# Performance work log

Hardware: AMD Instinct MI355X
Metric: run time of the kernel (lower is better)

The kernel has to match this reference:

```python
import jax, jax.numpy as jnp
import numpy as np

B = 16384
INPUT_DIM = 2048
HIDDEN = 1536
N_COMP = 256
N_LAYERS = 32
TOP_K = 4


def setup_inputs() -> dict:
    key = jax.random.key(0)
    ks = jax.random.split(key, 12)
    s_in = 1.0 / np.sqrt(INPUT_DIM)
    s_h = 1.0 / np.sqrt(HIDDEN)
    s_3 = 1.0 / np.sqrt(3)
    return {
        "x": jax.random.normal(ks[0], (B, INPUT_DIM), dtype=jnp.float32),
        "layer_idx": 3,
        "embed": jax.random.normal(ks[1], (N_LAYERS, INPUT_DIM), dtype=jnp.float32),
        "enc_w1": jax.random.uniform(ks[2], (INPUT_DIM, HIDDEN), jnp.float32, -s_in, s_in),
        "enc_b1": jax.random.uniform(ks[3], (HIDDEN,), jnp.float32, -s_in, s_in),
        "enc_w2": jax.random.uniform(ks[4], (HIDDEN, N_COMP), jnp.float32, -s_h, s_h),
        "enc_b2": jax.random.uniform(ks[5], (N_COMP,), jnp.float32, -s_h, s_h),
        "components": jax.random.normal(ks[6], (N_COMP, 3), dtype=jnp.float32),
        "dec_w1": jax.random.uniform(ks[7], (3, HIDDEN), jnp.float32, -s_3, s_3),
        "dec_b1": jax.random.uniform(ks[8], (HIDDEN,), jnp.float32, -s_3, s_3),
        "dec_w2": jax.random.uniform(ks[9], (HIDDEN, INPUT_DIM), jnp.float32, -s_h, s_h),
        "dec_b2": jax.random.uniform(ks[10], (INPUT_DIM,), jnp.float32, -s_h, s_h),
    }


def reference(x, layer_idx, embed, enc_w1, enc_b1, enc_w2, enc_b2,
              components, dec_w1, dec_b1, dec_w2, dec_b2):
    # x: (B, D). Add per-layer embedding row.
    x = x + embed[layer_idx]
    # Encoder MLP: Linear -> GELU (exact, erf-based like torch default) -> Linear
    h = jax.nn.gelu(x @ enc_w1 + enc_b1, approximate=False)
    logits = h @ enc_w2 + enc_b2                     # (B, C)
    # Top-k gated masked softmax: softmax over only the top_k logits per row.
    vals, idx = jax.lax.top_k(logits, TOP_K)         # (B, K), (B, K)
    w = jax.nn.softmax(vals, axis=-1)                # (B, K)
    # Sparse mix: equivalent to masked_fill(-inf) softmax @ components
    pts = jnp.einsum('bk,bkc->bc', w, components[idx])  # (B, 3)
    # Decoder MLP
    d = jax.nn.gelu(pts @ dec_w1 + dec_b1, approximate=False)
    decoded = d @ dec_w2 + dec_b2                    # (B, D)
    encoded = jnp.broadcast_to(components[None], (x.shape[0], N_COMP, 3))
    return encoded, decoded
```

## Files before the change

kernel.cpp:

```cpp
#include <hip/hip_runtime.h>


typedef float  f32x4  __attribute__((ext_vector_type(4)));
typedef short  short8 __attribute__((ext_vector_type(8)));
typedef int    i32x4  __attribute__((ext_vector_type(4)));

#define DEVINL __device__ __forceinline__

constexpr int  NB      = 16384;
constexpr int  IN_DIM  = 2048;
constexpr int  HID     = 1536;
constexpr int  NC      = 256;
constexpr long ENC_ELEMS = (long)NB * NC * 3;
constexpr float TAU  = 2e-5f;
constexpr float TAU1 = 1.5e-3f;
constexpr int  MAXR  = 64;
constexpr int  M2CAP = 2048;
constexpr int  NKT1 = IN_DIM / 32;
constexpr int  NKT2 = HID / 32;

constexpr float SCALE_X  = 3251.2f;
constexpr float SCALE_W1 = 1471325.0f;
constexpr float SCALE_H  = 4644.5714f;
constexpr float SCALE_W2 = 1274205.0f;
constexpr double INV_S1 = 1.0 / ((double)SCALE_X * (double)SCALE_W1);
constexpr double INV_S2 = 1.0 / ((double)SCALE_H * (double)SCALE_W2);
constexpr float C_DA     = 3.0f;
constexpr float SCALE_DA = 39.08f;
constexpr float SCALE_W2D = 4977.0f;
constexpr double INV_SD = 1.0 / ((double)SCALE_DA * (double)SCALE_W2D);

DEVINL unsigned short f2bf(float f) {
  unsigned int u = __builtin_bit_cast(unsigned int, f);
  u = u + 0x7fffu + ((u >> 16) & 1u);
  return (unsigned short)(u >> 16);
}
DEVINL float bf2f(unsigned short h) {
  unsigned int u = ((unsigned int)h) << 16;
  return __builtin_bit_cast(float, u);
}
DEVINL float gelu_f(float v) {
  return 0.5f * v * (1.0f + erff(v * 0.70710678118654752440f));
}
DEVINL void llds16(const void* g, void* l) {
  __builtin_amdgcn_global_load_lds(
      (const __attribute__((address_space(1))) void*)g,
      (__attribute__((address_space(3))) void*)l, 16, 0, 0);
}
DEVINL f32x4 mfma_bf16(short8 a, short8 b, f32x4 c) {
  return __builtin_amdgcn_mfma_f32_16x16x32_bf16(a, b, c, 0, 0, 0);
}
DEVINL i32x4 mfma_i8(i32x4 a, i32x4 b, i32x4 c) {
  return __builtin_amdgcn_mfma_i32_16x16x64_i8(a, b, c, 0, 0, 0);
}
DEVINL long packed_off(long tileIdx, int rowp, int kq, int e) {
  int slot = kq ^ ((rowp >> 1) & 3);
  return (tileIdx * 512 + rowp * 4 + slot) * 8 + e;
}
DEVINL int swz_idx(int rowp, int kq) {
  return (rowp * 4 + (kq ^ ((rowp >> 1) & 3))) * 8;
}
DEVINL long i8_off(long tile64, int rowp, int kin64) {
  return tile64 * 8192 + rowp * 64 + kin64;
}
DEVINL int quant16(float v, float scale) {
  int q = (int)lrintf(v * scale);
  if (q >  32512) q =  32512;
  if (q < -32512) q = -32512;
  return q;
}
DEVINL int quant8(float v, float scale) {
  int q = (int)lrintf(v * scale);
  if (q >  127) q =  127;
  if (q < -127) q = -127;
  return q;
}

__global__ __launch_bounds__(256) void mega_prep_kernel(
    const float* __restrict__ W1, const float* __restrict__ W2,
    const float* __restrict__ W2d, const float* __restrict__ b2d,
    const float* __restrict__ x, const float* __restrict__ embedMat,
    const int* __restrict__ liPtr,
    unsigned short* __restrict__ W1hT, unsigned short* __restrict__ W1lT,
    unsigned short* __restrict__ W2hT, unsigned short* __restrict__ W2lT,
    char* __restrict__ W1qh, char* __restrict__ W1ql,
    char* __restrict__ W2qh, char* __restrict__ W2ql,
    char* __restrict__ W2dq, float* __restrict__ badj,
    char* __restrict__ Xh, char* __restrict__ Xl,
    int* __restrict__ cnt, int* __restrict__ cnt2)
{
  constexpr int E0 = 3072;
  constexpr int E1 = E0 + 384;
  constexpr int E2 = E1 + 3072;
  constexpr int E3 = E2 + 8;
  constexpr int E4 = E3 + 8192;
  int b = blockIdx.x;
  int tid = threadIdx.x;
  __shared__ float t[32][33];

  if (b < E1) {
    const float* in; int N, nktB, nkt64; float qscale;
    unsigned short *oH, *oL; char *qH, *qL;
    int bx, by;
    if (b < E0) { in = W1;  N = HID; nktB = NKT1; nkt64 = IN_DIM / 64;
                  qscale = SCALE_W1; oH = W1hT; oL = W1lT; qH = W1qh; qL = W1ql;
                  bx = b % 48; by = b / 48; }
    else        { int bb = b - E0;
                  in = W2;  N = NC;  nktB = NKT2; nkt64 = HID / 64;
                  qscale = SCALE_W2; oH = W2hT; oL = W2lT; qH = W2qh; qL = W2ql;
                  bx = bb % 8; by = bb / 8; }
    int tx = tid & 31, ty = tid >> 5;
    int n0 = bx * 32, k0 = by * 32;
#pragma unroll
    for (int i = 0; i < 4; ++i)
      t[ty + i * 8][tx] = in[(long)(k0 + ty + i * 8) * N + n0 + tx];
    __syncthreads();
    int n = n0 + tx;
    int j = ty & 3;
    {
      long off = packed_off((long)(n >> 7) * nktB + (k0 >> 5), n & 127, j, 0);
      if (ty < 4) {
        short8 hv;
#pragma unroll
        for (int e = 0; e < 8; ++e) hv[e] = (short)f2bf(t[j * 8 + e][tx]);
        *(short8*)(oH + off) = hv;
      } else {
        short8 lv;
#pragma unroll
        for (int e = 0; e < 8; ++e) {
          float f = t[j * 8 + e][tx];
          lv[e] = (short)f2bf(f - bf2f(f2bf(f)));
        }
        *(short8*)(oL + off) = lv;
      }
    }
    {
      int kb = k0 + j * 8;
      long off = i8_off((long)(n >> 7) * nkt64 + (kb >> 6), n & 127, kb & 63);
      union { char b[8]; long v; } u;
      if (ty < 4) {
#pragma unroll
        for (int e = 0; e < 8; ++e) {
          int q = quant16(t[j * 8 + e][tx], qscale);
          int lo = (q << 24) >> 24;
          u.b[e] = (char)((q - lo) >> 8);
        }
        *(long*)(qH + off) = u.v;
      } else {
#pragma unroll
        for (int e = 0; e < 8; ++e) {
          int q = quant16(t[j * 8 + e][tx], qscale);
          u.b[e] = (char)((q << 24) >> 24);
        }
        *(long*)(qL + off) = u.v;
      }
    }
  } else if (b < E2) {
    int bb = b - E1;
    int bx = bb % 64, by = bb / 64;
    int tx = tid & 31, ty = tid >> 5;
    int n0 = bx * 32, k0 = by * 32;
#pragma unroll
    for (int i = 0; i < 4; ++i)
      t[ty + i * 8][tx] = W2d[(long)(k0 + ty + i * 8) * IN_DIM + n0 + tx];
    __syncthreads();
    if (ty < 4) {
      int n = n0 + tx;
      int kb = k0 + ty * 8;
      long off = i8_off((long)(n >> 7) * (HID / 64) + (kb >> 6), n & 127, kb & 63);
      union { char b[8]; long v; } u;
#pragma unroll
      for (int e = 0; e < 8; ++e)
        u.b[e] = (char)quant8(t[ty * 8 + e][tx], SCALE_W2D);
      *(long*)(W2dq + off) = u.v;
    }
  } else if (b < E3) {
    int j = (b - E2) * 256 + tid;
    float s = 0.f;
    for (int k = 0; k < HID; ++k) s += W2d[(long)k * IN_DIM + j];
    badj[j] = b2d[j] + C_DA * s;
  } else if (b < E4) {
    long g = (long)(b - E3) * 256 + tid;
    int row = (int)(g >> 7);
    int k0 = ((int)(g & 127)) * 16;
    int li = liPtr[0];
    const float* xr = x + (long)row * IN_DIM + k0;
    const float* er = embedMat + (long)li * IN_DIM + k0;
    union { char b[16]; i32x4 v; } hu, lu;
#pragma unroll
    for (int c = 0; c < 4; ++c) {
      f32x4 a = *(const f32x4*)(xr + c * 4);
      f32x4 e = *(const f32x4*)(er + c * 4);
#pragma unroll
      for (int jj = 0; jj < 4; ++jj) {
        int q = quant16(a[jj] + e[jj], SCALE_X);
        int lo = (q << 24) >> 24;
        hu.b[c * 4 + jj] = (char)((q - lo) >> 8);
        lu.b[c * 4 + jj] = (char)lo;
      }
    }
    long off = i8_off((long)(row >> 7) * (IN_DIM / 64) + (k0 >> 6), row & 127, k0 & 63);
    *(i32x4*)(Xh + off) = hu.v;
    *(i32x4*)(Xl + off) = lu.v;
  } else {
    if (tid == 0) { *cnt = 0; *cnt2 = 0; }
  }
}

template<int OUT, int PRODUCTS>
__global__ __launch_bounds__(256, 2) void gemm_i8_kernel(
    const char* __restrict__ Ah, const char* __restrict__ Al,
    const char* __restrict__ Bh, const char* __restrict__ Bl,
    int nkt64, const float* __restrict__ bias, double invScale,
    float* __restrict__ Cf, long ldc,
    char* __restrict__ Qh, char* __restrict__ Ql, int nktOut64, float outScale,
    int nbn)
{
  __shared__ alignas(16) char sAh[8192];
  __shared__ alignas(16) char sAl[PRODUCTS == 3 ? 8192 : 16];
  __shared__ alignas(16) char sBh[8192];
  __shared__ alignas(16) char sBl[PRODUCTS == 3 ? 8192 : 16];
  __shared__ float sBias[128];

  int tid = threadIdx.x;
  int nwg = gridDim.x, q = nwg >> 3, b0 = blockIdx.x;
  int sw = (b0 & 7) * q + (b0 >> 3);
  int bm = sw / nbn, bn = sw % nbn;

  if (tid < 128) sBias[tid] = bias[bn * 128 + tid];

  int wid = tid >> 6, lane = tid & 63;
  int wm = wid >> 1, wn = wid & 1;
  int l15 = lane & 15, kq = lane >> 4;

  i32x4 accH[4][4] = {};
  i32x4 accM[4][4] = {};

  for (int kt = 0; kt < nkt64; ++kt) {
    __syncthreads();
    {
      const char* g0 = Ah + ((long)(bm * nkt64 + kt)) * 8192 + tid * 16;
      llds16(g0, sAh + tid * 16); llds16(g0 + 4096, sAh + 4096 + tid * 16);
      const char* g2 = Bh + ((long)(bn * nkt64 + kt)) * 8192 + tid * 16;
      llds16(g2, sBh + tid * 16); llds16(g2 + 4096, sBh + 4096 + tid * 16);
      if constexpr (PRODUCTS == 3) {
        const char* g1 = Al + ((long)(bm * nkt64 + kt)) * 8192 + tid * 16;
        llds16(g1, sAl + tid * 16); llds16(g1 + 4096, sAl + 4096 + tid * 16);
        const char* g3 = Bl + ((long)(bn * nkt64 + kt)) * 8192 + tid * 16;
        llds16(g3, sBl + tid * 16); llds16(g3 + 4096, sBl + 4096 + tid * 16);
      }
    }
    __syncthreads();

    i32x4 bhf[4], blf[4];
#pragma unroll
    for (int n = 0; n < 4; ++n) {
      int off = (wn * 64 + n * 16 + l15) * 64 + kq * 16;
      bhf[n] = *(const i32x4*)&sBh[off];
      if constexpr (PRODUCTS == 3) blf[n] = *(const i32x4*)&sBl[off];
    }
#pragma unroll
    for (int m = 0; m < 4; ++m) {
      int off = (wm * 64 + m * 16 + l15) * 64 + kq * 16;
      i32x4 ahf = *(const i32x4*)&sAh[off];
      i32x4 alf;
      if constexpr (PRODUCTS == 3) alf = *(const i32x4*)&sAl[off];
#pragma unroll
      for (int n = 0; n < 4; ++n) {
        accH[m][n] = mfma_i8(ahf, bhf[n], accH[m][n]);
        if constexpr (PRODUCTS == 3) {
          accM[m][n] = mfma_i8(alf, bhf[n], accM[m][n]);
          accM[m][n] = mfma_i8(ahf, blf[n], accM[m][n]);
        }
      }
    }
  }

#pragma unroll
  for (int m = 0; m < 4; ++m) {
#pragma unroll
    for (int n = 0; n < 4; ++n) {
      int  gcol = bn * 128 + wn * 64 + n * 16 + l15;
      float bb  = sBias[wn * 64 + n * 16 + l15];
#pragma unroll
      for (int r = 0; r < 4; ++r) {
        long grow = (long)bm * 128 + wm * 64 + m * 16 + kq * 4 + r;
        double dv;
        if constexpr (PRODUCTS == 3)
          dv = (double)accH[m][n][r] * 65536.0 + (double)accM[m][n][r] * 256.0;
        else
          dv = (double)accH[m][n][r];
        float v = (float)(dv * invScale) + bb;
        if constexpr (OUT == 0) {
          Cf[grow * ldc + gcol] = v;
        } else {
          v = gelu_f(v);
          int qq = quant16(v, outScale);
          int lo = (qq << 24) >> 24;
          long off = i8_off((long)(grow >> 7) * nktOut64 + (gcol >> 6),
                            (int)(grow & 127), gcol & 63);
          Qh[off] = (char)((qq - lo) >> 8);
          Ql[off] = (char)lo;
        }
      }
    }
  }
}

template<bool SPLIT, int OUT_MODE, bool GELU, int KU>
__global__ __launch_bounds__(256) void gemm2_kernel(
    const unsigned short* __restrict__ Ah, const unsigned short* __restrict__ Al,
    const unsigned short* __restrict__ Bh, const unsigned short* __restrict__ Bl,
    int nkt, const float* __restrict__ bias, float* __restrict__ Cf,
    unsigned short* __restrict__ Ch, unsigned short* __restrict__ Cl,
    long ldc, int nktOut, int nbn, const int* __restrict__ mrows, int mcap)
{
  __shared__ alignas(16) unsigned short sAh[4096 * KU];
  __shared__ alignas(16) unsigned short sAl[SPLIT ? 4096 * KU : 8];
  __shared__ alignas(16) unsigned short sBh[4096 * KU];
  __shared__ alignas(16) unsigned short sBl[SPLIT ? 4096 * KU : 8];
  __shared__ float sBias[128];

  int tid = threadIdx.x;
  int nwg = gridDim.x, q = nwg >> 3, b0 = blockIdx.x;
  int sw = (b0 & 7) * q + (b0 >> 3);
  int bm = sw / nbn, bn = sw % nbn;

  if (mrows) {
    int v = *mrows; if (v > mcap) v = mcap;
    if (bm * 128 >= v) return;
  }

  if (tid < 128) sBias[tid] = bias[bn * 128 + tid];

  int wid = tid >> 6, lane = tid & 63;
  int wm = wid >> 1, wn = wid & 1;
  int l15 = lane & 15, kq = lane >> 4;

  f32x4 acc[4][4] = {};

  for (int kt = 0; kt < nkt; kt += KU) {
    __syncthreads();
#pragma unroll
    for (int u = 0; u < KU; ++u) {
      {
        const char* gA = (const char*)Ah + ((long)(bm * nkt + kt + u)) * 8192 + tid * 16;
        llds16(gA,        (char*)sAh + u * 8192 + tid * 16);
        llds16(gA + 4096, (char*)sAh + u * 8192 + 4096 + tid * 16);
      }
      if constexpr (SPLIT) {
        const char* gA = (const char*)Al + ((long)(bm * nkt + kt + u)) * 8192 + tid * 16;
        llds16(gA,        (char*)sAl + u * 8192 + tid * 16);
        llds16(gA + 4096, (char*)sAl + u * 8192 + 4096 + tid * 16);
      }
      {
        const char* gB = (const char*)Bh + ((long)(bn * nkt + kt + u)) * 8192 + tid * 16;
        llds16(gB,        (char*)sBh + u * 8192 + tid * 16);
        llds16(gB + 4096, (char*)sBh + u * 8192 + 4096 + tid * 16);
      }
      if constexpr (SPLIT) {
        const char* gB = (const char*)Bl + ((long)(bn * nkt + kt + u)) * 8192 + tid * 16;
        llds16(gB,        (char*)sBl + u * 8192 + tid * 16);
        llds16(gB + 4096, (char*)sBl + u * 8192 + 4096 + tid * 16);
      }
    }
    __syncthreads();

#pragma unroll
    for (int u = 0; u < KU; ++u) {
      short8 bh[4], bl[4];
#pragma unroll
      for (int n = 0; n < 4; ++n) {
        int idx = u * 4096 + swz_idx(wn * 64 + n * 16 + l15, kq);
        bh[n] = *(const short8*)&sBh[idx];
        if constexpr (SPLIT) bl[n] = *(const short8*)&sBl[idx];
      }
#pragma unroll
      for (int m = 0; m < 4; ++m) {
        int idx = u * 4096 + swz_idx(wm * 64 + m * 16 + l15, kq);
        short8 ah = *(const short8*)&sAh[idx];
        short8 al;
        if constexpr (SPLIT) al = *(const short8*)&sAl[idx];
#pragma unroll
        for (int n = 0; n < 4; ++n) {
          acc[m][n] = mfma_bf16(ah, bh[n], acc[m][n]);
          if constexpr (SPLIT) {
            acc[m][n] = mfma_bf16(al, bh[n], acc[m][n]);
            acc[m][n] = mfma_bf16(ah, bl[n], acc[m][n]);
          }
        }
      }
    }
  }

#pragma unroll
  for (int m = 0; m < 4; ++m) {
#pragma unroll
    for (int n = 0; n < 4; ++n) {
      int  gcol = bn * 128 + wn * 64 + n * 16 + l15;
      float bb  = sBias[wn * 64 + n * 16 + l15];
#pragma unroll
      for (int r = 0; r < 4; ++r) {
        long grow = (long)bm * 128 + wm * 64 + m * 16 + kq * 4 + r;
        float v = acc[m][n][r] + bb;
        if constexpr (GELU) v = gelu_f(v);
        if constexpr (OUT_MODE == 0) {
          Cf[grow * ldc + gcol] = v;
        } else {
          int Mt = (int)(grow >> 7), rowpo = (int)(grow & 127);
          int Kt = gcol >> 5, kqo = (gcol >> 3) & 3, e = gcol & 7;
          long off = packed_off((long)Mt * nktOut + Kt, rowpo, kqo, e);
          unsigned short hb = f2bf(v);
          Ch[off] = hb;
          Cl[off] = f2bf(v - bf2f(hb));
        }
      }
    }
  }
}

__global__ __launch_bounds__(256) void topk_screen_kernel(
    const float* __restrict__ logits, const float* __restrict__ comp,
    float* __restrict__ pts, float* __restrict__ encOut,
    int* __restrict__ cnt2, int* __restrict__ list2,
    int* __restrict__ rescueCnt, int* __restrict__ rescueList)
{
  int wid = threadIdx.x >> 6, lane = threadIdx.x & 63;
  long row = (long)blockIdx.x * 4 + wid;
  f32x4 v4 = *(const f32x4*)(logits + row * NC + lane * 4);
  float a[4] = {v4[0], v4[1], v4[2], v4[3]};

  float tv[5]; int ti[5];
#pragma unroll
  for (int t = 0; t < 5; ++t) {
    float lv = a[0]; int li = lane * 4;
#pragma unroll
    for (int i = 1; i < 4; ++i)
      if (a[i] > lv) { lv = a[i]; li = lane * 4 + i; }
#pragma unroll
    for (int off = 32; off >= 1; off >>= 1) {
      float ov = __shfl_xor(lv, off);
      int   oi = __shfl_xor(li, off);
      if (ov > lv || (ov == lv && oi < li)) { lv = ov; li = oi; }
    }
    tv[t] = lv; ti[t] = li;
    if (t < 4 && (li >> 2) == lane) a[li & 3] = -INFINITY;
  }

  bool flag = (tv[3] - tv[4]) < TAU1;
  if (!flag) {
    float m = tv[0], w[4], s = 0.f;
#pragma unroll
    for (int t = 0; t < 4; ++t) { w[t] = expf(tv[t] - m); s += w[t]; }
    float inv = 1.0f / s;
    if (lane < 3) {
      float p = 0.f;
#pragma unroll
      for (int t = 0; t < 4; ++t) p += w[t] * inv * comp[ti[t] * 3 + lane];
      pts[row * 3 + lane] = p;
    }
  } else if (lane == 0) {
    int pos = atomicAdd(cnt2, 1);
    if (pos < M2CAP) list2[pos] = (int)row;
    else { int rp = atomicAdd(rescueCnt, 1); rescueList[rp] = (int)row; }
  }

  const f32x4* cv = (const f32x4*)comp;
  f32x4* ov = (f32x4*)encOut + (long)blockIdx.x * 768;
  for (int j = threadIdx.x; j < 768; j += 256)
    ov[j] = cv[j % 192];
}

__global__ __launch_bounds__(256) void gather_kernel(
    const float* __restrict__ x, const float* __restrict__ embedMat,
    const int* __restrict__ liPtr, const int* __restrict__ cnt2,
    const int* __restrict__ list2,
    unsigned short* __restrict__ A2h, unsigned short* __restrict__ A2l)
{
  int i = blockIdx.x;
  int c2 = *cnt2; if (c2 > M2CAP) c2 = M2CAP;
  if (i >= c2) return;
  int row = list2[i];
  int li = liPtr[0];
  int t = threadIdx.x;
  int k0 = t * 8;
  const float* xr = x + (long)row * IN_DIM + k0;
  const float* er = embedMat + (long)li * IN_DIM + k0;
  short8 hv, lv;
#pragma unroll
  for (int c = 0; c < 2; ++c) {
    f32x4 a = *(const f32x4*)(xr + c * 4);
    f32x4 e = *(const f32x4*)(er + c * 4);
#pragma unroll
    for (int jj = 0; jj < 4; ++jj) {
      float f = a[jj] + e[jj];
      unsigned short hb = f2bf(f);
      hv[c * 4 + jj] = (short)hb;
      lv[c * 4 + jj] = (short)f2bf(f - bf2f(hb));
    }
  }
  long off = packed_off((long)(i >> 7) * NKT1 + (k0 >> 5), i & 127, (k0 >> 3) & 3, 0);
  *(short8*)(A2h + off) = hv;
  *(short8*)(A2l + off) = lv;
}

__global__ __launch_bounds__(256) void topk_final_kernel(
    const float* __restrict__ logits2, const float* __restrict__ comp,
    const int* __restrict__ cnt2, const int* __restrict__ list2,
    float* __restrict__ pts, int* __restrict__ rescueCnt, int* __restrict__ rescueList)
{
  int wid = threadIdx.x >> 6, lane = threadIdx.x & 63;
  int slot = blockIdx.x * 4 + wid;
  int c2 = *cnt2; if (c2 > M2CAP) c2 = M2CAP;
  if (slot >= c2) return;
  int row = list2[slot];
  f32x4 v4 = *(const f32x4*)(logits2 + (long)slot * NC + lane * 4);
  float a[4] = {v4[0], v4[1], v4[2], v4[3]};

  float tv[5]; int ti[5];
#pragma unroll
  for (int t = 0; t < 5; ++t) {
    float lv = a[0]; int li = lane * 4;
#pragma unroll
    for (int i = 1; i < 4; ++i)
      if (a[i] > lv) { lv = a[i]; li = lane * 4 + i; }
#pragma unroll
    for (int off = 32; off >= 1; off >>= 1) {
      float ov = __shfl_xor(lv, off);
      int   oi = __shfl_xor(li, off);
      if (ov > lv || (ov == lv && oi < li)) { lv = ov; li = oi; }
    }
    tv[t] = lv; ti[t] = li;
    if (t < 4 && (li >> 2) == lane) a[li & 3] = -INFINITY;
  }

  float m = tv[0], w[4], s = 0.f;
#pragma unroll
  for (int t = 0; t < 4; ++t) { w[t] = expf(tv[t] - m); s += w[t]; }
  float inv = 1.0f / s;
  if (lane < 3) {
    float p = 0.f;
#pragma unroll
    for (int t = 0; t < 4; ++t) p += w[t] * inv * comp[ti[t] * 3 + lane];
    pts[(long)row * 3 + lane] = p;
  }
  if (lane == 0 && (tv[3] - tv[4]) < TAU) {
    int pos = atomicAdd(rescueCnt, 1);
    rescueList[pos] = row;
  }
}

__global__ __launch_bounds__(256) void rescue_h1_kernel(
    const float* __restrict__ x, const float* __restrict__ embedMat,
    const int* __restrict__ liPtr, const float* __restrict__ W1,
    const int* __restrict__ cnt, const int* __restrict__ list,
    double* __restrict__ partial)
{
  int b = blockIdx.x;
  int s = b / 24, rem = b % 24;
  int cc = rem >> 2, kp = rem & 3;
  int n = *cnt;
  if (s >= n || s >= MAXR) return;
  int row = list[s];
  __shared__ double xd[512];
  int tid = threadIdx.x;
  int li = liPtr[0];
  int k0 = kp * 512;
  for (int j = tid; j < 512; j += 256)
    xd[j] = (double)x[(long)row * IN_DIM + k0 + j]
          + (double)embedMat[(long)li * IN_DIM + k0 + j];
  __syncthreads();
  int c = cc * 256 + tid;
  const float* wp = W1 + (long)k0 * HID + c;
  double s0 = 0, s1 = 0, s2 = 0, s3 = 0;
  for (int k = 0; k < 512; k += 4) {
    s0 += xd[k]     * (double)wp[(long)k * HID];
    s1 += xd[k + 1] * (double)wp[(long)(k + 1) * HID];
    s2 += xd[k + 2] * (double)wp[(long)(k + 2) * HID];
    s3 += xd[k + 3] * (double)wp[(long)(k + 3) * HID];
  }
  partial[((long)(s * 6 + cc) * 4 + kp) * 256 + tid] = (s0 + s1) + (s2 + s3);
}

__global__ __launch_bounds__(256) void rescue_logits_kernel(
    const float* __restrict__ b1, const float* __restrict__ W2,
    const float* __restrict__ b2, const float* __restrict__ comp,
    const int* __restrict__ cnt, const int* __restrict__ list,
    const double* __restrict__ partial, float* __restrict__ pts)
{
  int s = blockIdx.x;
  int n = *cnt;
  if (s >= n || s >= MAXR) return;
  __shared__ double hd[HID];
  __shared__ double ld[NC];
  int tid = threadIdx.x;
  for (int cc = 0; cc < 6; ++cc) {
    long base = ((long)(s * 6 + cc) * 4) * 256 + tid;
    double v = (double)b1[cc * 256 + tid]
             + ((partial[base] + partial[base + 256])
              + (partial[base + 512] + partial[base + 768]));
    hd[cc * 256 + tid] = 0.5 * v * (1.0 + erf(v * 0.70710678118654752440));
  }
  __syncthreads();
  {
    const float* wp = W2 + tid;
    double a0 = 0, a1 = 0, a2 = 0, a3 = 0;
    for (int k = 0; k < HID; k += 4) {
      a0 += hd[k]     * (double)wp[(long)k * NC];
      a1 += hd[k + 1] * (double)wp[(long)(k + 1) * NC];
      a2 += hd[k + 2] * (double)wp[(long)(k + 2) * NC];
      a3 += hd[k + 3] * (double)wp[(long)(k + 3) * NC];
    }
    ld[tid] = (double)b2[tid] + ((a0 + a1) + (a2 + a3));
  }
  __syncthreads();
  if (tid == 0) {
    int row = list[s];
    int idx[4]; double val[4];
    unsigned long long mask[4] = {0, 0, 0, 0};
    for (int t = 0; t < 4; ++t) {
      double bv = -1e300; int bi = 0;
      for (int j = 0; j < NC; ++j) {
        if ((mask[j >> 6] >> (j & 63)) & 1ull) continue;
        if (ld[j] > bv) { bv = ld[j]; bi = j; }
      }
      idx[t] = bi; val[t] = bv; mask[bi >> 6] |= 1ull << (bi & 63);
    }
    double m = val[0], w[4], sum = 0;
    for (int t = 0; t < 4; ++t) { w[t] = exp(val[t] - m); sum += w[t]; }
    for (int c = 0; c < 3; ++c) {
      double p = 0;
      for (int t = 0; t < 4; ++t) p += (w[t] / sum) * (double)comp[idx[t] * 3 + c];
      pts[(long)row * 3 + c] = (float)p;
    }
  }
}

__global__ __launch_bounds__(256) void rescue_slow_kernel(
    const float* __restrict__ x, const float* __restrict__ embedMat,
    const int* __restrict__ liPtr, const float* __restrict__ W1,
    const float* __restrict__ b1, const float* __restrict__ W2,
    const float* __restrict__ b2, const float* __restrict__ comp,
    float* __restrict__ pts, const int* __restrict__ cnt, const int* __restrict__ list)
{
  __shared__ double xd[IN_DIM];
  __shared__ double hd[HID];
  __shared__ double ld[NC];
  int tid = threadIdx.x;
  int li = liPtr[0];
  int n = *cnt;
  for (int it = MAXR + blockIdx.x; it < n; it += gridDim.x) {
    int row = list[it];
    const float* xr = x + (long)row * IN_DIM;
    const float* er = embedMat + (long)li * IN_DIM;
    for (int j = tid; j < IN_DIM; j += 256)
      xd[j] = (double)xr[j] + (double)er[j];
    __syncthreads();
    for (int c = tid; c < HID; c += 256) {
      double s0 = 0, s1 = 0, s2 = 0, s3 = 0;
      const float* wp = W1 + c;
      for (int k = 0; k < IN_DIM; k += 4) {
        s0 += xd[k]     * (double)wp[(long)k * HID];
        s1 += xd[k + 1] * (double)wp[(long)(k + 1) * HID];
        s2 += xd[k + 2] * (double)wp[(long)(k + 2) * HID];
        s3 += xd[k + 3] * (double)wp[(long)(k + 3) * HID];
      }
      double s = (double)b1[c] + ((s0 + s1) + (s2 + s3));
      hd[c] = 0.5 * s * (1.0 + erf(s * 0.70710678118654752440));
    }
    __syncthreads();
    {
      int c = tid;
      double s0 = 0, s1 = 0, s2 = 0, s3 = 0;
      const float* wp = W2 + c;
      for (int k = 0; k < HID; k += 4) {
        s0 += hd[k]     * (double)wp[(long)k * NC];
        s1 += hd[k + 1] * (double)wp[(long)(k + 1) * NC];
        s2 += hd[k + 2] * (double)wp[(long)(k + 2) * NC];
        s3 += hd[k + 3] * (double)wp[(long)(k + 3) * NC];
      }
      ld[c] = (double)b2[c] + ((s0 + s1) + (s2 + s3));
    }
    __syncthreads();
    if (tid == 0) {
      int idx[4]; double val[4];
      unsigned long long mask[4] = {0, 0, 0, 0};
      for (int t = 0; t < 4; ++t) {
        double bv = -1e300; int bi = 0;
        for (int j = 0; j < NC; ++j) {
          if ((mask[j >> 6] >> (j & 63)) & 1ull) continue;
          if (ld[j] > bv) { bv = ld[j]; bi = j; }
        }
        idx[t] = bi; val[t] = bv; mask[bi >> 6] |= 1ull << (bi & 63);
      }
      double m = val[0], w[4], s = 0;
      for (int t = 0; t < 4; ++t) { w[t] = exp(val[t] - m); s += w[t]; }
      for (int c = 0; c < 3; ++c) {
        double p = 0;
        for (int t = 0; t < 4; ++t) p += (w[t] / s) * (double)comp[idx[t] * 3 + c];
        pts[(long)row * 3 + c] = (float)p;
      }
    }
    __syncthreads();
  }
}

__global__ __launch_bounds__(256) void dec_a_kernel(
    const float* __restrict__ pts, const float* __restrict__ W1d,
    const float* __restrict__ b1d, char* __restrict__ dq)
{
  for (long u = blockIdx.x; u < (long)NB * 6; u += gridDim.x) {
    int  j = (int)(u % 6) * 256 + threadIdx.x;
    long b = u / 6;
    const float* p = pts + b * 3;
    float s = fmaf(p[0], W1d[j], fmaf(p[1], W1d[HID + j], fmaf(p[2], W1d[2 * HID + j], b1d[j])));
    float d = gelu_f(s);
    int q = quant8(d - C_DA, SCALE_DA);
    int Mt = (int)(b >> 7), rowp = (int)(b & 127);
    dq[i8_off((long)Mt * (HID / 64) + (j >> 6), rowp, j & 63)] = (char)q;
  }
}

extern "C" void kernel_launch(void* const* d_in, const int* in_sizes, int n_in,
                              void* d_out, int out_size, void* d_ws, size_t ws_size,
                              hipStream_t stream) {
  const float* x     = (const float*)d_in[0];
  const int*   liPtr = (const int*)  d_in[1];
  const float* embed = (const float*)d_in[2];
  const float* W1    = (const float*)d_in[3];
  const float* b1    = (const float*)d_in[4];
  const float* W2    = (const float*)d_in[5];
  const float* b2    = (const float*)d_in[6];
  const float* comp  = (const float*)d_in[7];
  const float* W1d   = (const float*)d_in[8];
  const float* b1d   = (const float*)d_in[9];
  const float* W2d   = (const float*)d_in[10];
  const float* b2d   = (const float*)d_in[11];
  float* out = (float*)d_out;

  char* w = (char*)d_ws;
  unsigned short* W1hT = (unsigned short*)(w);
  unsigned short* W1lT = (unsigned short*)(w + 6291456);
  unsigned short* W2hT = (unsigned short*)(w + 12582912);
  unsigned short* W2lT = (unsigned short*)(w + 13369344);
  char*  W2dq = w + 14155776;
  float* badj = (float*)(w + 17301504);
  char* W1qh = w + 20447232;
  char* W1ql = w + 23592960;
  char* W2qh = w + 26738688;
  char* W2ql = w + 27131904;
  char* Xqh = w + 27525120;
  char* Xql = w + 61079552;
  char* Hqh = w + 94633984;
  char* Hql = w + 119799808;
  float* logits = (float*)(w + 144965632);
  unsigned short* A2h = (unsigned short*)(w + 161742848);
  unsigned short* A2l = (unsigned short*)(w + 178520064);
  unsigned short* H2h = (unsigned short*)(w + 195297280);
  unsigned short* H2l = (unsigned short*)(w + 207880192);
  float* logits2 = (float*)(w + 220463104);
  char*  dq = w + 27525120;
  float* pts   = (float*)(w + 224657408);
  int*   cnt   = (int*)  (w + 224854016);
  int*   cnt2  = (int*)  (w + 224854272);
  int*   list  = (int*)  (w + 224854528);
  int*   list2 = (int*)  (w + 224920064);
  double* partial = (double*)(w + 224936448);

  mega_prep_kernel<<<14729, 256, 0, stream>>>(
      W1, W2, W2d, b2d, x, embed, liPtr,
      W1hT, W1lT, W2hT, W2lT, W1qh, W1ql, W2qh, W2ql,
      W2dq, badj, Xqh, Xql, cnt, cnt2);

  gemm_i8_kernel<1, 3><<<(NB / 128) * (HID / 128), 256, 0, stream>>>(
      Xqh, Xql, W1qh, W1ql, IN_DIM / 64, b1, INV_S1,
      nullptr, 0, Hqh, Hql, HID / 64, SCALE_H, HID / 128);
  gemm_i8_kernel<0, 3><<<(NB / 128) * (NC / 128), 256, 0, stream>>>(
      Hqh, Hql, W2qh, W2ql, HID / 64, b2, INV_S2,
      logits, NC, nullptr, nullptr, 0, 0.f, NC / 128);

  topk_screen_kernel<<<NB / 4, 256, 0, stream>>>(logits, comp, pts, out, cnt2, list2, cnt, list);

  gather_kernel<<<M2CAP, 256, 0, stream>>>(x, embed, liPtr, cnt2, list2, A2h, A2l);
  gemm2_kernel<true, 2, true, 4><<<(M2CAP / 128) * (HID / 128), 256, 0, stream>>>(
      A2h, A2l, W1hT, W1lT, NKT1, b1, nullptr, H2h, H2l, 0, NKT2, HID / 128, cnt2, M2CAP);
  gemm2_kernel<true, 0, false, 4><<<(M2CAP / 128) * (NC / 128), 256, 0, stream>>>(
      H2h, H2l, W2hT, W2lT, NKT2, b2, logits2, nullptr, nullptr, NC, 0, NC / 128, cnt2, M2CAP);
  topk_final_kernel<<<M2CAP / 4, 256, 0, stream>>>(logits2, comp, cnt2, list2, pts, cnt, list);

  rescue_h1_kernel<<<MAXR * 24, 256, 0, stream>>>(x, embed, liPtr, W1, cnt, list, partial);
  rescue_logits_kernel<<<MAXR, 256, 0, stream>>>(b1, W2, b2, comp, cnt, list, partial, pts);
  rescue_slow_kernel<<<64, 256, 0, stream>>>(x, embed, liPtr, W1, b1, W2, b2, comp, pts, cnt, list);

  dec_a_kernel<<<3072, 256, 0, stream>>>(pts, W1d, b1d, dq);
  gemm_i8_kernel<0, 1><<<(NB / 128) * (IN_DIM / 128), 256, 0, stream>>>(
      dq, nullptr, W2dq, nullptr, HID / 64, badj, INV_SD,
      out + ENC_ELEMS, IN_DIM, nullptr, nullptr, 0, 0.f, IN_DIM / 128);
}
```

Baseline: 712.6 us.

## Split decoder bias column-sum across blocks and shrink rescue capacity

The column-sum of W2d over the hidden dimension, which was done by only 8 blocks each looping over all 1536 rows, is now split into 16 partial sums across 128 blocks. The decoder GEMM reduces the 16 partials while loading its bias tile. Separately, the screening threshold TAU1 is tightened and the capacity of the exact-recompute path M2CAP is halved, so the second-pass GEMMs over flagged rows launch half as many blocks. The tighter threshold and smaller cap risk overflowing the rescue list or flagging fewer near-tie rows, which could change top-k correctness on harder inputs.

```diff
diff --git a/kernel.cpp b/kernel.cpp
--- a/kernel.cpp
+++ b/kernel.cpp
@@ -13,9 +13,9 @@
 constexpr int  NC      = 256;
 constexpr long ENC_ELEMS = (long)NB * NC * 3;
 constexpr float TAU  = 2e-5f;
-constexpr float TAU1 = 1.5e-3f;
+constexpr float TAU1 = 8e-4f;
 constexpr int  MAXR  = 64;
-constexpr int  M2CAP = 2048;
+constexpr int  M2CAP = 1024;
 constexpr int  NKT1 = IN_DIM / 32;
 constexpr int  NKT2 = HID / 32;
 
@@ -78,21 +78,21 @@
 
 __global__ __launch_bounds__(256) void mega_prep_kernel(
     const float* __restrict__ W1, const float* __restrict__ W2,
-    const float* __restrict__ W2d, const float* __restrict__ b2d,
+    const float* __restrict__ W2d,
     const float* __restrict__ x, const float* __restrict__ embedMat,
     const int* __restrict__ liPtr,
     unsigned short* __restrict__ W1hT, unsigned short* __restrict__ W1lT,
     unsigned short* __restrict__ W2hT, unsigned short* __restrict__ W2lT,
     char* __restrict__ W1qh, char* __restrict__ W1ql,
     char* __restrict__ W2qh, char* __restrict__ W2ql,
-    char* __restrict__ W2dq, float* __restrict__ badj,
+    char* __restrict__ W2dq, float* __restrict__ biasPart,
     char* __restrict__ Xh, char* __restrict__ Xl,
     int* __restrict__ cnt, int* __restrict__ cnt2)
 {
   constexpr int E0 = 3072;
   constexpr int E1 = E0 + 384;
   constexpr int E2 = E1 + 3072;
-  constexpr int E3 = E2 + 8;
+  constexpr int E3 = E2 + 128;
   constexpr int E4 = E3 + 8192;
   int b = blockIdx.x;
   int tid = threadIdx.x;
@@ -175,10 +175,13 @@
       *(long*)(W2dq + off) = u.v;
     }
   } else if (b < E3) {
-    int j = (b - E2) * 256 + tid;
+    int bb = b - E2;
+    int p = bb >> 3, jb = bb & 7;
+    int j = jb * 256 + tid;
     float s = 0.f;
-    for (int k = 0; k < HID; ++k) s += W2d[(long)k * IN_DIM + j];
-    badj[j] = b2d[j] + C_DA * s;
+    int kBeg = p * (HID / 16), kEnd = kBeg + (HID / 16);
+    for (int k = kBeg; k < kEnd; ++k) s += W2d[(long)k * IN_DIM + j];
+    biasPart[(long)p * IN_DIM + j] = s;
   } else if (b < E4) {
     long g = (long)(b - E3) * 256 + tid;
     int row = (int)(g >> 7);
@@ -207,12 +210,12 @@
   }
 }
 
-template<int OUT, int PRODUCTS>
+template<int OUT, int PRODUCTS, bool BIASRED>
 __global__ __launch_bounds__(256, 2) void gemm_i8_kernel(
     const char* __restrict__ Ah, const char* __restrict__ Al,
     const char* __restrict__ Bh, const char* __restrict__ Bl,
-    int nkt64, const float* __restrict__ bias, double invScale,
-    float* __restrict__ Cf, long ldc,
+    int nkt64, const float* __restrict__ bias, const float* __restrict__ biasPart,
+    double invScale, float* __restrict__ Cf, long ldc,
     char* __restrict__ Qh, char* __restrict__ Ql, int nktOut64, float outScale,
     int nbn)
 {
@@ -227,7 +230,17 @@
   int sw = (b0 & 7) * q + (b0 >> 3);
   int bm = sw / nbn, bn = sw % nbn;
 
-  if (tid < 128) sBias[tid] = bias[bn * 128 + tid];
+  if (tid < 128) {
+    int col = bn * 128 + tid;
+    float bb = bias[col];
+    if constexpr (BIASRED) {
+      float s = 0.f;
+#pragma unroll
+      for (int p = 0; p < 16; ++p) s += biasPart[(long)p * IN_DIM + col];
+      bb += C_DA * s;
+    }
+    sBias[tid] = bb;
+  }
 
   int wid = tid >> 6, lane = tid & 63;
   int wm = wid >> 1, wn = wid & 1;
@@ -744,7 +757,7 @@
   unsigned short* W2hT = (unsigned short*)(w + 12582912);
   unsigned short* W2lT = (unsigned short*)(w + 13369344);
   char*  W2dq = w + 14155776;
-  float* badj = (float*)(w + 17301504);
+  float* biasPart = (float*)(w + 17301504);
   char* W1qh = w + 20447232;
   char* W1ql = w + 23592960;
   char* W2qh = w + 26738688;
@@ -767,16 +780,16 @@
   int*   list2 = (int*)  (w + 224920064);
   double* partial = (double*)(w + 224936448);
 
-  mega_prep_kernel<<<14729, 256, 0, stream>>>(
-      W1, W2, W2d, b2d, x, embed, liPtr,
+  mega_prep_kernel<<<14849, 256, 0, stream>>>(
+      W1, W2, W2d, x, embed, liPtr,
       W1hT, W1lT, W2hT, W2lT, W1qh, W1ql, W2qh, W2ql,
-      W2dq, badj, Xqh, Xql, cnt, cnt2);
-
-  gemm_i8_kernel<1, 3><<<(NB / 128) * (HID / 128), 256, 0, stream>>>(
-      Xqh, Xql, W1qh, W1ql, IN_DIM / 64, b1, INV_S1,
+      W2dq, biasPart, Xqh, Xql, cnt, cnt2);
+
+  gemm_i8_kernel<1, 3, false><<<(NB / 128) * (HID / 128), 256, 0, stream>>>(
+      Xqh, Xql, W1qh, W1ql, IN_DIM / 64, b1, nullptr, INV_S1,
       nullptr, 0, Hqh, Hql, HID / 64, SCALE_H, HID / 128);
-  gemm_i8_kernel<0, 3><<<(NB / 128) * (NC / 128), 256, 0, stream>>>(
-      Hqh, Hql, W2qh, W2ql, HID / 64, b2, INV_S2,
+  gemm_i8_kernel<0, 3, false><<<(NB / 128) * (NC / 128), 256, 0, stream>>>(
+      Hqh, Hql, W2qh, W2ql, HID / 64, b2, nullptr, INV_S2,
       logits, NC, nullptr, nullptr, 0, 0.f, NC / 128);
 
   topk_screen_kernel<<<NB / 4, 256, 0, stream>>>(logits, comp, pts, out, cnt2, list2, cnt, list);
@@ -793,7 +806,7 @@
   rescue_slow_kernel<<<64, 256, 0, stream>>>(x, embed, liPtr, W1, b1, W2, b2, comp, pts, cnt, list);
 
   dec_a_kernel<<<3072, 256, 0, stream>>>(pts, W1d, b1d, dq);
-  gemm_i8_kernel<0, 1><<<(NB / 128) * (IN_DIM / 128), 256, 0, stream>>>(
-      dq, nullptr, W2dq, nullptr, HID / 64, badj, INV_SD,
+  gemm_i8_kernel<0, 1, true><<<(NB / 128) * (IN_DIM / 128), 256, 0, stream>>>(
+      dq, nullptr, W2dq, nullptr, HID / 64, b2d, biasPart, INV_SD,
       out + ENC_ELEMS, IN_DIM, nullptr, nullptr, 0, 0.f, IN_DIM / 128);
 }
```

After: 664.9 us. 1.07x faster.
